# Kernel tuning notes

Hardware: AMD Instinct MI355X
Metric: run time of the kernel (lower is better)

Reference implementation:

```python
import jax, jax.numpy as jnp
import numpy as np

N_GRAPHS = 64


def gcn_conv(x, W, b, src, dst, n_nodes):
    """PyG GCNConv: add self-loops, symmetric D^-1/2 (A+I) D^-1/2 normalization,
    linear transform, scatter-add aggregation at target nodes, plus bias."""
    xw = x @ W  # [N, out]  transform before propagate (PyG order)
    loop = jnp.arange(n_nodes, dtype=src.dtype)
    rows = jnp.concatenate([src, loop])  # message sources
    cols = jnp.concatenate([dst, loop])  # message targets
    deg = jax.ops.segment_sum(jnp.ones_like(cols, dtype=xw.dtype), cols,
                              num_segments=n_nodes)
    dinv = jnp.where(deg > 0, jax.lax.rsqrt(deg), 0.0)
    norm = dinv[rows] * dinv[cols]  # [E+N]
    msgs = norm[:, None] * xw[rows]  # gather + scale
    out = jax.ops.segment_sum(msgs, cols, num_segments=n_nodes)  # scatter-add
    return out + b


def global_mean_pool(x, batch, n_graphs):
    sums = jax.ops.segment_sum(x, batch, num_segments=n_graphs)
    cnts = jax.ops.segment_sum(jnp.ones((x.shape[0],), x.dtype), batch,
                               num_segments=n_graphs)
    return sums / jnp.maximum(cnts, 1.0)[:, None]


def setup_inputs() -> dict:
    key = jax.random.key(0)
    k1, k2, k3, k4, k5, k6 = jax.random.split(key, 6)
    N, E = 50000, 800000
    d_in, d_hid, d_out = 128, 128, 64
    x = jax.random.normal(k1, (N, d_in), dtype=jnp.float32)
    edge_index = jax.random.randint(k2, (2, E), 0, N, dtype=jnp.int64)
    batch = jnp.sort(jax.random.randint(k3, (N,), 0, N_GRAPHS, dtype=jnp.int64))
    # Glorot-ish init for GCN weights, zero bias (PyG default)
    W1 = jax.random.normal(k4, (d_in, d_hid), dtype=jnp.float32) / np.sqrt(d_in)
    b1 = jnp.zeros((d_hid,), jnp.float32)
    W2 = jax.random.normal(k5, (d_hid, d_out), dtype=jnp.float32) / np.sqrt(d_hid)
    b2 = jnp.zeros((d_out,), jnp.float32)
    return {"x": x, "edge_index": edge_index, "batch": batch,
            "W1": W1, "b1": b1, "W2": W2, "b2": b2}


def reference(x, edge_index, batch, W1, b1, W2, b2):
    n_nodes = x.shape[0]
    src, dst = edge_index[0], edge_index[1]
    h = jax.nn.relu(gcn_conv(x, W1, b1, src, dst, n_nodes))
    h = gcn_conv(h, W2, b2, src, dst, n_nodes)
    return global_mean_pool(h, batch, N_GRAPHS)
```

## Files before the change

### kernel.cpp

```cpp
#include <hip/hip_runtime.h>
#include <hip/hip_fp16.h>

typedef __attribute__((ext_vector_type(8))) short bf16x8;
typedef __attribute__((ext_vector_type(4))) float f32x4;

__device__ __forceinline__ unsigned short f2bf(float f) {
  unsigned u = __float_as_uint(f);
  u += 0x7FFFu + ((u >> 16) & 1u);
  return (unsigned short)(u >> 16);
}
__device__ __forceinline__ float bflo(unsigned u) { return __uint_as_float(u << 16); }
__device__ __forceinline__ float bfhi(unsigned u) { return __uint_as_float(u & 0xFFFF0000u); }
__device__ __forceinline__ float unpackw(unsigned pk) {
  return __half2float(__ushort_as_half((unsigned short)(pk >> 16)));
}

template <int CO, bool AF32>
__device__ __forceinline__ void gemm_body(const void* __restrict__ Aptr,
                                          const float* __restrict__ W,
                                          unsigned short* __restrict__ Y, int N,
                                          int bid, int tid, unsigned short* Wl) {
  constexpr int K = 128;
  constexpr int SP = K + 8;
  for (int i = tid; i < K * CO; i += 256) {
    int k = i / CO, n = i % CO;
    Wl[n * SP + k] = f2bf(W[i]);
  }
  __syncthreads();

  const int lane = tid & 63;
  const int quad = lane >> 4, l16 = lane & 15;
  const int mbase = bid * 64 + (tid >> 6) * 16;
  const int arow = min(mbase + l16, N - 1);

  bf16x8 afrag[4];
  if constexpr (AF32) {
    const float* A = (const float*)Aptr + (size_t)arow * K;
#pragma unroll
    for (int ks = 0; ks < 4; ks++) {
      const float4* p = (const float4*)(A + ks * 32 + quad * 8);
      float4 f0 = p[0], f1 = p[1];
      afrag[ks] = (bf16x8){(short)f2bf(f0.x), (short)f2bf(f0.y), (short)f2bf(f0.z), (short)f2bf(f0.w),
                           (short)f2bf(f1.x), (short)f2bf(f1.y), (short)f2bf(f1.z), (short)f2bf(f1.w)};
    }
  } else {
    const unsigned short* A = (const unsigned short*)Aptr + (size_t)arow * K;
#pragma unroll
    for (int ks = 0; ks < 4; ks++) afrag[ks] = *(const bf16x8*)(A + ks * 32 + quad * 8);
  }

#pragma unroll
  for (int ct = 0; ct < CO / 16; ct++) {
    f32x4 acc = {0.0f, 0.0f, 0.0f, 0.0f};
#pragma unroll
    for (int ks = 0; ks < 4; ks++) {
      bf16x8 b = *(const bf16x8*)(&Wl[(ct * 16 + l16) * SP + ks * 32 + quad * 8]);
      acc = __builtin_amdgcn_mfma_f32_16x16x32_bf16(afrag[ks], b, acc, 0, 0, 0);
    }
#pragma unroll
    for (int reg = 0; reg < 4; reg++) {
      int node = mbase + quad * 4 + reg;
      if (node < N) Y[(size_t)node * CO + ct * 16 + l16] = f2bf(acc[reg]);
    }
  }
}

__global__ __launch_bounds__(256) void k_mega1(const float* __restrict__ x,
                                               const float* __restrict__ W1,
                                               unsigned short* __restrict__ xw1b, int N,
                                               const int* __restrict__ src,
                                               const int* __restrict__ dst,
                                               int* __restrict__ cnt,
                                               unsigned short* __restrict__ colsrc, int E,
                                               const int* __restrict__ batch,
                                               int* __restrict__ firstIdx,
                                               int gM, int gE4) {
  __shared__ unsigned short Wl[128 * 136];
  const int bid = blockIdx.x, tid = threadIdx.x;
  if (bid < gM) {
    gemm_body<128, true>(x, W1, xw1b, N, bid, tid, Wl);
  } else if (bid < gM + gE4) {
    int e0 = (bid - gM) * 1024 + tid * 4;
    if (e0 + 3 < E) {
      int4 d4 = *(const int4*)(dst + e0);
      int4 s4 = *(const int4*)(src + e0);
      int r;
      r = atomicAdd(&cnt[d4.x], 1); if (r < 64) colsrc[(d4.x << 6) + r] = (unsigned short)s4.x;
      r = atomicAdd(&cnt[d4.y], 1); if (r < 64) colsrc[(d4.y << 6) + r] = (unsigned short)s4.y;
      r = atomicAdd(&cnt[d4.z], 1); if (r < 64) colsrc[(d4.z << 6) + r] = (unsigned short)s4.z;
      r = atomicAdd(&cnt[d4.w], 1); if (r < 64) colsrc[(d4.w << 6) + r] = (unsigned short)s4.w;
    } else {
      for (int e = e0; e < E; e++) {
        int d = dst[e];
        int r = atomicAdd(&cnt[d], 1);
        if (r < 64) colsrc[(d << 6) + r] = (unsigned short)src[e];
      }
    }
  } else {
    int n = (bid - gM - gE4) * 256 + tid;
    if (n < N) {
      int b = batch[n];
      if (n == 0 || batch[n - 1] != b) firstIdx[b] = n + 1;
    }
  }
}

__global__ __launch_bounds__(256) void k_agg128(const unsigned short* __restrict__ xwb,
                                                const int* __restrict__ cnt,
                                                const unsigned short* __restrict__ colsrc,
                                                const float* __restrict__ bias,
                                                unsigned short* __restrict__ out, int N,
                                                const int* __restrict__ firstIdx,
                                                const float* __restrict__ b2,
                                                float* __restrict__ invc,
                                                float* __restrict__ gout, int gA) {
  const int bid = blockIdx.x, tid = threadIdx.x;
  if (bid == gA) {
    if (tid < 64) {
      int raw = firstIdx[tid];
      int fi = (raw > 0) ? raw - 1 : 0x7FFFFFFF;
      int m = fi;
#pragma unroll
      for (int d = 1; d < 64; d <<= 1) {
        int t = __shfl_down(m, d, 64);
        if (tid + d < 64) m = min(m, t);
      }
      int nxtm = __shfl_down(m, 1, 64);
      int nxt = (tid == 63) ? N : min(nxtm, N);
      int c = (fi == 0x7FFFFFFF) ? 0 : (nxt - fi);
      invc[tid] = 1.0f / fmaxf((float)c, 1.0f);
    }
    for (int i = tid; i < 64 * 64; i += 256) gout[i] = b2[i & 63];
    return;
  }
  const int lane = tid & 63;
  const int gl = lane & 15;
  const int grp = lane >> 4;
  const int wv = tid >> 6;
  const int v = bid * 16 + wv * 4 + grp;
  const int vc = min(v, N - 1);

  const int c = cnt[vc];
  const int jc = (v < N) ? min(c, 64) : 0;
  const float dv = rsqrtf((float)(c + 1));

  float acc[8];
  {
    const float d2 = dv * dv;
    uint4 s = *(const uint4*)((const char*)xwb + (((size_t)vc << 8) | (gl << 4)));
    acc[0] = d2 * bflo(s.x); acc[1] = d2 * bfhi(s.x);
    acc[2] = d2 * bflo(s.y); acc[3] = d2 * bfhi(s.y);
    acc[4] = d2 * bflo(s.z); acc[5] = d2 * bfhi(s.z);
    acc[6] = d2 * bflo(s.w); acc[7] = d2 * bfhi(s.w);
  }

  const int gbase = grp << 4;
  for (int base = 0; __any(base < jc); base += 16) {
    unsigned pk0 = 0u;
    if (base + gl < jc) {
      int s = colsrc[(vc << 6) + base + gl];
      float ws = rsqrtf((float)(cnt[s] + 1)) * dv;
      pk0 = (unsigned)s | ((unsigned)__half_as_ushort(__float2half_rn(ws)) << 16);
    }
    int mv = jc - base;
    mv = mv < 0 ? 0 : (mv > 16 ? 16 : mv);
    int mm = max(mv, __shfl_xor(mv, 16, 64));
    mm = max(mm, __shfl_xor(mm, 32, 64));
    const int rp = (mm + 7) & ~7;
    for (int t = 0; t < rp; t += 8) {
      uint4 rbuf[8];
      float wbuf[8];
#pragma unroll
      for (int r = 0; r < 8; r++) {
        unsigned pk = (unsigned)__shfl((int)pk0, gbase + t + r, 64);
        wbuf[r] = unpackw(pk);
        rbuf[r] = *(const uint4*)((const char*)xwb + (((pk & 0xFFFFu) << 8) | (gl << 4)));
      }
#pragma unroll
      for (int r = 0; r < 8; r++) {
        const float w = wbuf[r];
        const uint4 rr = rbuf[r];
        acc[0] += w * bflo(rr.x); acc[1] += w * bfhi(rr.x);
        acc[2] += w * bflo(rr.y); acc[3] += w * bfhi(rr.y);
        acc[4] += w * bflo(rr.z); acc[5] += w * bfhi(rr.z);
        acc[6] += w * bflo(rr.w); acc[7] += w * bfhi(rr.w);
      }
    }
  }

  if (v < N) {
    float4 b0 = ((const float4*)bias)[gl * 2];
    float4 b1 = ((const float4*)bias)[gl * 2 + 1];
    float a0 = fmaxf(acc[0] + b0.x, 0.f), a1 = fmaxf(acc[1] + b0.y, 0.f);
    float a2 = fmaxf(acc[2] + b0.z, 0.f), a3 = fmaxf(acc[3] + b0.w, 0.f);
    float a4 = fmaxf(acc[4] + b1.x, 0.f), a5 = fmaxf(acc[5] + b1.y, 0.f);
    float a6 = fmaxf(acc[6] + b1.z, 0.f), a7 = fmaxf(acc[7] + b1.w, 0.f);
    uint4 st;
    st.x = (unsigned)f2bf(a0) | ((unsigned)f2bf(a1) << 16);
    st.y = (unsigned)f2bf(a2) | ((unsigned)f2bf(a3) << 16);
    st.z = (unsigned)f2bf(a4) | ((unsigned)f2bf(a5) << 16);
    st.w = (unsigned)f2bf(a6) | ((unsigned)f2bf(a7) << 16);
    *(uint4*)((char*)out + (((size_t)v << 8) | (gl << 4))) = st;
  }
}

__global__ __launch_bounds__(256) void k_gemm2(const unsigned short* __restrict__ A,
                                               const float* __restrict__ W,
                                               unsigned short* __restrict__ Y, int N) {
  __shared__ unsigned short Wl[64 * 136];
  gemm_body<64, false>(A, W, Y, N, blockIdx.x, threadIdx.x, Wl);
}

__global__ __launch_bounds__(256) void k_aggpool(const unsigned short* __restrict__ xwb,
                                                 const int* __restrict__ cnt,
                                                 const unsigned short* __restrict__ colsrc,
                                                 const int* __restrict__ batch,
                                                 const float* __restrict__ invc,
                                                 float* __restrict__ out, int N) {
  __shared__ float sAcc[4][64];
  const int tid = threadIdx.x;
  const int lane = tid & 63;
  const int gl = lane & 7;
  const int grp = lane >> 3;
  const int wv = tid >> 6;
  const int v = blockIdx.x * 32 + wv * 8 + grp;
  const int vc = min(v, N - 1);

  const int c = cnt[vc];
  const int jc = (v < N) ? min(c, 64) : 0;
  const float dv = rsqrtf((float)(c + 1));
  const int b = batch[vc];

  float acc[8];
  {
    const float d2 = dv * dv;
    uint4 s = *(const uint4*)((const char*)xwb + (((size_t)vc << 7) | (gl << 4)));
    acc[0] = d2 * bflo(s.x); acc[1] = d2 * bfhi(s.x);
    acc[2] = d2 * bflo(s.y); acc[3] = d2 * bfhi(s.y);
    acc[4] = d2 * bflo(s.z); acc[5] = d2 * bfhi(s.z);
    acc[6] = d2 * bflo(s.w); acc[7] = d2 * bfhi(s.w);
  }

  const int gbase = grp << 3;
  for (int base = 0; __any(base < jc); base += 8) {
    unsigned pk0 = 0u;
    if (base + gl < jc) {
      int s = colsrc[(vc << 6) + base + gl];
      float ws = rsqrtf((float)(cnt[s] + 1)) * dv;
      pk0 = (unsigned)s | ((unsigned)__half_as_ushort(__float2half_rn(ws)) << 16);
    }
    uint4 rbuf[8];
    float wbuf[8];
#pragma unroll
    for (int r = 0; r < 8; r++) {
      unsigned pk = (unsigned)__shfl((int)pk0, gbase + r, 64);
      wbuf[r] = unpackw(pk);
      rbuf[r] = *(const uint4*)((const char*)xwb + (((pk & 0xFFFFu) << 7) | (gl << 4)));
    }
#pragma unroll
    for (int r = 0; r < 8; r++) {
      const float w = wbuf[r];
      const uint4 rr = rbuf[r];
      acc[0] += w * bflo(rr.x); acc[1] += w * bfhi(rr.x);
      acc[2] += w * bflo(rr.y); acc[3] += w * bfhi(rr.y);
      acc[4] += w * bflo(rr.z); acc[5] += w * bfhi(rr.z);
      acc[6] += w * bflo(rr.w); acc[7] += w * bfhi(rr.w);
    }
  }

  const float sc = (v < N) ? invc[b] : 0.0f;
#pragma unroll
  for (int k = 0; k < 8; k++) acc[k] *= sc;

  const int v0 = blockIdx.x * 32;
  const bool uniform = (v0 + 31 < N) && (batch[v0] == batch[v0 + 31]);
  if (uniform) {
#pragma unroll
    for (int d = 8; d < 64; d <<= 1)
#pragma unroll
      for (int k = 0; k < 8; k++) acc[k] += __shfl_xor(acc[k], d, 64);
    if (grp == 0) {
      *(float4*)&sAcc[wv][gl * 8] = make_float4(acc[0], acc[1], acc[2], acc[3]);
      *(float4*)&sAcc[wv][gl * 8 + 4] = make_float4(acc[4], acc[5], acc[6], acc[7]);
    }
    __syncthreads();
    if (wv == 0) {
      float t = sAcc[0][lane] + sAcc[1][lane] + sAcc[2][lane] + sAcc[3][lane];
      atomicAdd(&out[batch[v0] * 64 + lane], t);
    }
  } else if (v < N) {
#pragma unroll
    for (int k = 0; k < 8; k++) atomicAdd(&out[b * 64 + gl * 8 + k], acc[k]);
  }
}


extern "C" void kernel_launch(void* const* d_in, const int* in_sizes, int n_in,
                              void* d_out, int out_size, void* d_ws, size_t ws_size,
                              hipStream_t stream) {
  const float* x     = (const float*)d_in[0];
  const int*   ei    = (const int*)d_in[1];
  const int*   batch = (const int*)d_in[2];
  const float* W1    = (const float*)d_in[3];
  const float* b1    = (const float*)d_in[4];
  const float* W2    = (const float*)d_in[5];
  const float* b2    = (const float*)d_in[6];

  const int N = in_sizes[2];
  const int E = in_sizes[1] / 2;
  const int* src  = ei;
  const int* dstv = ei + E;

  unsigned short* xw1b = (unsigned short*)d_ws;
  unsigned short* h1b  = xw1b + (size_t)N * 128;
  unsigned short* xw2b = xw1b;
  int*   cnt     = (int*)(h1b + (size_t)N * 128);
  int*   firstIdx= cnt + N;
  float* invc    = (float*)(firstIdx + 64);
  unsigned short* colsrc = (unsigned short*)(invc + 64);
  float* outp    = (float*)d_out;

  hipMemsetAsync(cnt, 0, (size_t)(N + 64) * sizeof(int), stream);

  const int gM  = (N + 63) / 64;
  const int gE4 = (E + 1023) / 1024;
  const int gN  = (N + 255) / 256;
  const int gA1 = (N + 15) / 16;
  const int gA2 = (N + 31) / 32;

  k_mega1<<<gM + gE4 + gN, 256, 0, stream>>>(x, W1, xw1b, N, src, dstv, cnt,
                                             colsrc, E, batch, firstIdx, gM, gE4);

  k_agg128<<<gA1 + 1, 256, 0, stream>>>(xw1b, cnt, colsrc, b1, h1b, N,
                                        firstIdx, b2, invc, outp, gA1);

  k_gemm2<<<gM, 256, 0, stream>>>(h1b, W2, xw2b, N);
  k_aggpool<<<gA2, 256, 0, stream>>>(xw2b, cnt, colsrc, batch, invc, outp, N);
}
```

Baseline: 202.8 us.

## Reorder second layer to pool before applying W2, dropping the node-level GEMM

Uses linearity to aggregate and mean-pool the 128-wide hidden features per graph first, then multiply the 64x128 pooled matrix by W2 in a small final kernel. This removes the N-row second GEMM and its intermediate write/read. In exchange the second aggregation gathers 128-wide rows instead of 64-wide ones, doubling gather bytes, and adds fp32 atomics into a larger staging buffer plus an extra small kernel.

```diff
diff --git a/kernel.cpp b/kernel.cpp
--- a/kernel.cpp
+++ b/kernel.cpp
@@ -109,35 +109,13 @@
                                                 const int* __restrict__ cnt,
                                                 const unsigned short* __restrict__ colsrc,
                                                 const float* __restrict__ bias,
-                                                unsigned short* __restrict__ out, int N,
-                                                const int* __restrict__ firstIdx,
-                                                const float* __restrict__ b2,
-                                                float* __restrict__ invc,
-                                                float* __restrict__ gout, int gA) {
-  const int bid = blockIdx.x, tid = threadIdx.x;
-  if (bid == gA) {
-    if (tid < 64) {
-      int raw = firstIdx[tid];
-      int fi = (raw > 0) ? raw - 1 : 0x7FFFFFFF;
-      int m = fi;
-#pragma unroll
-      for (int d = 1; d < 64; d <<= 1) {
-        int t = __shfl_down(m, d, 64);
-        if (tid + d < 64) m = min(m, t);
-      }
-      int nxtm = __shfl_down(m, 1, 64);
-      int nxt = (tid == 63) ? N : min(nxtm, N);
-      int c = (fi == 0x7FFFFFFF) ? 0 : (nxt - fi);
-      invc[tid] = 1.0f / fmaxf((float)c, 1.0f);
-    }
-    for (int i = tid; i < 64 * 64; i += 256) gout[i] = b2[i & 63];
-    return;
-  }
+                                                unsigned short* __restrict__ out, int N) {
+  const int tid = threadIdx.x;
   const int lane = tid & 63;
   const int gl = lane & 15;
   const int grp = lane >> 4;
   const int wv = tid >> 6;
-  const int v = bid * 16 + wv * 4 + grp;
+  const int v = blockIdx.x * 16 + wv * 4 + grp;
   const int vc = min(v, N - 1);
 
   const int c = cnt[vc];
@@ -204,93 +182,126 @@
   }
 }
 
-__global__ __launch_bounds__(256) void k_gemm2(const unsigned short* __restrict__ A,
-                                               const float* __restrict__ W,
-                                               unsigned short* __restrict__ Y, int N) {
-  __shared__ unsigned short Wl[64 * 136];
-  gemm_body<64, false>(A, W, Y, N, blockIdx.x, threadIdx.x, Wl);
-}
-
-__global__ __launch_bounds__(256) void k_aggpool(const unsigned short* __restrict__ xwb,
-                                                 const int* __restrict__ cnt,
-                                                 const unsigned short* __restrict__ colsrc,
-                                                 const int* __restrict__ batch,
-                                                 const float* __restrict__ invc,
-                                                 float* __restrict__ out, int N) {
-  __shared__ float sAcc[4][64];
+__global__ __launch_bounds__(256) void k_aggpool2(const unsigned short* __restrict__ h1b,
+                                                  const int* __restrict__ cnt,
+                                                  const unsigned short* __restrict__ colsrc,
+                                                  const int* __restrict__ batch,
+                                                  float* __restrict__ stage, int N) {
+  __shared__ float sAcc[4][128];
   const int tid = threadIdx.x;
   const int lane = tid & 63;
-  const int gl = lane & 7;
-  const int grp = lane >> 3;
+  const int gl = lane & 15;
+  const int grp = lane >> 4;
   const int wv = tid >> 6;
-  const int v = blockIdx.x * 32 + wv * 8 + grp;
+  const int v = blockIdx.x * 16 + wv * 4 + grp;
   const int vc = min(v, N - 1);
 
   const int c = cnt[vc];
   const int jc = (v < N) ? min(c, 64) : 0;
   const float dv = rsqrtf((float)(c + 1));
-  const int b = batch[vc];
 
   float acc[8];
   {
-    const float d2 = dv * dv;
-    uint4 s = *(const uint4*)((const char*)xwb + (((size_t)vc << 7) | (gl << 4)));
+    const float d2 = (v < N) ? dv * dv : 0.0f;
+    uint4 s = *(const uint4*)((const char*)h1b + (((size_t)vc << 8) | (gl << 4)));
     acc[0] = d2 * bflo(s.x); acc[1] = d2 * bfhi(s.x);
     acc[2] = d2 * bflo(s.y); acc[3] = d2 * bfhi(s.y);
     acc[4] = d2 * bflo(s.z); acc[5] = d2 * bfhi(s.z);
     acc[6] = d2 * bflo(s.w); acc[7] = d2 * bfhi(s.w);
   }
 
-  const int gbase = grp << 3;
-  for (int base = 0; __any(base < jc); base += 8) {
+  const int gbase = grp << 4;
+  for (int base = 0; __any(base < jc); base += 16) {
     unsigned pk0 = 0u;
     if (base + gl < jc) {
       int s = colsrc[(vc << 6) + base + gl];
       float ws = rsqrtf((float)(cnt[s] + 1)) * dv;
       pk0 = (unsigned)s | ((unsigned)__half_as_ushort(__float2half_rn(ws)) << 16);
     }
-    uint4 rbuf[8];
-    float wbuf[8];
-#pragma unroll
-    for (int r = 0; r < 8; r++) {
-      unsigned pk = (unsigned)__shfl((int)pk0, gbase + r, 64);
-      wbuf[r] = unpackw(pk);
-      rbuf[r] = *(const uint4*)((const char*)xwb + (((pk & 0xFFFFu) << 7) | (gl << 4)));
-    }
-#pragma unroll
-    for (int r = 0; r < 8; r++) {
-      const float w = wbuf[r];
-      const uint4 rr = rbuf[r];
-      acc[0] += w * bflo(rr.x); acc[1] += w * bfhi(rr.x);
-      acc[2] += w * bflo(rr.y); acc[3] += w * bfhi(rr.y);
-      acc[4] += w * bflo(rr.z); acc[5] += w * bfhi(rr.z);
-      acc[6] += w * bflo(rr.w); acc[7] += w * bfhi(rr.w);
-    }
-  }
-
-  const float sc = (v < N) ? invc[b] : 0.0f;
-#pragma unroll
-  for (int k = 0; k < 8; k++) acc[k] *= sc;
-
-  const int v0 = blockIdx.x * 32;
-  const bool uniform = (v0 + 31 < N) && (batch[v0] == batch[v0 + 31]);
+    int mv = jc - base;
+    mv = mv < 0 ? 0 : (mv > 16 ? 16 : mv);
+    int mm = max(mv, __shfl_xor(mv, 16, 64));
+    mm = max(mm, __shfl_xor(mm, 32, 64));
+    const int rp = (mm + 7) & ~7;
+    for (int t = 0; t < rp; t += 8) {
+      uint4 rbuf[8];
+      float wbuf[8];
+#pragma unroll
+      for (int r = 0; r < 8; r++) {
+        unsigned pk = (unsigned)__shfl((int)pk0, gbase + t + r, 64);
+        wbuf[r] = unpackw(pk);
+        rbuf[r] = *(const uint4*)((const char*)h1b + (((pk & 0xFFFFu) << 8) | (gl << 4)));
+      }
+#pragma unroll
+      for (int r = 0; r < 8; r++) {
+        const float w = wbuf[r];
+        const uint4 rr = rbuf[r];
+        acc[0] += w * bflo(rr.x); acc[1] += w * bfhi(rr.x);
+        acc[2] += w * bflo(rr.y); acc[3] += w * bfhi(rr.y);
+        acc[4] += w * bflo(rr.z); acc[5] += w * bfhi(rr.z);
+        acc[6] += w * bflo(rr.w); acc[7] += w * bfhi(rr.w);
+      }
+    }
+  }
+
+  const int v0 = blockIdx.x * 16;
+  const bool uniform = (v0 + 15 < N) && (batch[v0] == batch[v0 + 15]);
   if (uniform) {
 #pragma unroll
-    for (int d = 8; d < 64; d <<= 1)
+    for (int d = 16; d < 64; d <<= 1)
 #pragma unroll
       for (int k = 0; k < 8; k++) acc[k] += __shfl_xor(acc[k], d, 64);
     if (grp == 0) {
-      *(float4*)&sAcc[wv][gl * 8] = make_float4(acc[0], acc[1], acc[2], acc[3]);
-      *(float4*)&sAcc[wv][gl * 8 + 4] = make_float4(acc[4], acc[5], acc[6], acc[7]);
+#pragma unroll
+      for (int k = 0; k < 8; k++) sAcc[wv][gl * 8 + k] = acc[k];
     }
     __syncthreads();
     if (wv == 0) {
-      float t = sAcc[0][lane] + sAcc[1][lane] + sAcc[2][lane] + sAcc[3][lane];
-      atomicAdd(&out[batch[v0] * 64 + lane], t);
+      const int g = batch[v0];
+      float t0 = sAcc[0][lane] + sAcc[1][lane] + sAcc[2][lane] + sAcc[3][lane];
+      float t1 = sAcc[0][lane + 64] + sAcc[1][lane + 64] + sAcc[2][lane + 64] + sAcc[3][lane + 64];
+      atomicAdd(&stage[g * 128 + lane], t0);
+      atomicAdd(&stage[g * 128 + lane + 64], t1);
     }
   } else if (v < N) {
-#pragma unroll
-    for (int k = 0; k < 8; k++) atomicAdd(&out[b * 64 + gl * 8 + k], acc[k]);
+    const int b = batch[vc];
+#pragma unroll
+    for (int k = 0; k < 8; k++) atomicAdd(&stage[b * 128 + gl * 8 + k], acc[k]);
+  }
+}
+
+__global__ void k_wout(const float* __restrict__ stage, const int* __restrict__ firstIdx,
+                       const float* __restrict__ W2, const float* __restrict__ b2,
+                       float* __restrict__ out, int N) {
+  __shared__ float denom[64];
+  __shared__ float red[256];
+  const int tid = threadIdx.x;
+  const int g = blockIdx.x;
+  if (tid < 64) {
+    int raw = firstIdx[tid];
+    int fi = (raw > 0) ? raw - 1 : 0x7FFFFFFF;
+    int m = fi;
+#pragma unroll
+    for (int d = 1; d < 64; d <<= 1) {
+      int t = __shfl_down(m, d, 64);
+      if (tid + d < 64) m = min(m, t);
+    }
+    int nxtm = __shfl_down(m, 1, 64);
+    int nxt = (tid == 63) ? N : min(nxtm, N);
+    int c = (fi == 0x7FFFFFFF) ? 0 : (nxt - fi);
+    denom[tid] = fmaxf((float)c, 1.0f);
+  }
+  __syncthreads();
+  const int j = tid & 63, kc = tid >> 6;
+  float p = 0.0f;
+#pragma unroll 8
+  for (int k = kc * 32; k < kc * 32 + 32; k++)
+    p += stage[g * 128 + k] * W2[k * 64 + j];
+  red[tid] = p;
+  __syncthreads();
+  if (tid < 64) {
+    float t = red[tid] + red[tid + 64] + red[tid + 128] + red[tid + 192];
+    out[g * 64 + tid] = t / denom[g] + b2[tid];
   }
 }
 
@@ -313,27 +324,25 @@
 
   unsigned short* xw1b = (unsigned short*)d_ws;
   unsigned short* h1b  = xw1b + (size_t)N * 128;
-  unsigned short* xw2b = xw1b;
   int*   cnt     = (int*)(h1b + (size_t)N * 128);
   int*   firstIdx= cnt + N;
-  float* invc    = (float*)(firstIdx + 64);
-  unsigned short* colsrc = (unsigned short*)(invc + 64);
+  float* stage   = (float*)(firstIdx + 64);
+  unsigned short* colsrc = (unsigned short*)(stage + 64 * 128);
   float* outp    = (float*)d_out;
 
-  hipMemsetAsync(cnt, 0, (size_t)(N + 64) * sizeof(int), stream);
+  hipMemsetAsync(cnt, 0, (size_t)(N + 64 + 64 * 128) * sizeof(int), stream);
 
   const int gM  = (N + 63) / 64;
   const int gE4 = (E + 1023) / 1024;
   const int gN  = (N + 255) / 256;
   const int gA1 = (N + 15) / 16;
-  const int gA2 = (N + 31) / 32;
 
   k_mega1<<<gM + gE4 + gN, 256, 0, stream>>>(x, W1, xw1b, N, src, dstv, cnt,
                                              colsrc, E, batch, firstIdx, gM, gE4);
 
-  k_agg128<<<gA1 + 1, 256, 0, stream>>>(xw1b, cnt, colsrc, b1, h1b, N,
-                                        firstIdx, b2, invc, outp, gA1);
-
-  k_gemm2<<<gM, 256, 0, stream>>>(h1b, W2, xw2b, N);
-  k_aggpool<<<gA2, 256, 0, stream>>>(xw2b, cnt, colsrc, batch, invc, outp, N);
-}
+  k_agg128<<<gA1, 256, 0, stream>>>(xw1b, cnt, colsrc, b1, h1b, N);
+
+  k_aggpool2<<<gA1, 256, 0, stream>>>(h1b, cnt, colsrc, batch, stage, N);
+
+  k_wout<<<64, 256, 0, stream>>>(stage, firstIdx, W2, b2, outp, N);
+}
```

Measured after the change: 190.2 us, median of 2. 6.2% less time.
